# Performance work log

Hardware: AMD Instinct MI355X
Metric: run time of the kernel (lower is better)

## Reference

```python
import jax, jax.numpy as jnp
import numpy as np

B, H, W = 4, 240, 320
J = 2            # BONE_NUM
F = 64           # FEATURE_CHANNELS
R = 32           # voxel RESOLUTION
THRESH = 0.7
BIG = 1e30
# channel layout from init_hp(): nocs | mask | loc | pose | skin | conf | feature
NE = 3
ME = NE + 1
LE = ME + J * 3
PE = LE + J * 3
SE = PE + J + 2
CE = SE + J
FE = CE + F      # = 86 total channels


def _rodrigues(r):
    # axis-angle [..., 3] -> rotation matrix [..., 3, 3]
    ang = jnp.sqrt(jnp.sum(r * r, -1, keepdims=True)) + 1e-8
    ax = r / ang
    x, y, z = ax[..., 0], ax[..., 1], ax[..., 2]
    zz = jnp.zeros_like(x)
    K = jnp.stack([zz, -z, y, z, zz, -x, -y, x, zz], -1).reshape(r.shape[:-1] + (3, 3))
    c = jnp.cos(ang)[..., None]
    s = jnp.sin(ang)[..., None]
    return jnp.eye(3, dtype=r.dtype) + s * K + (1.0 - c) * (K @ K)


def setup_inputs() -> dict:
    key = jax.random.key(0)
    return {"output": jax.random.normal(key, (B, FE, H, W), dtype=jnp.float32)}


def _forward(output):
    mask = jax.nn.sigmoid(output[:, NE])                      # [B,H,W]
    conf = output[:, SE:CE]                                   # [B,J,H,W]
    score = jax.nn.sigmoid(conf) * mask[:, None]
    score = score / (score.reshape(B, J, -1).sum(-1)[:, :, None, None] + 1e-5)

    def vote(jmap):  # weighted joint voting, joint map detached as in torch
        jm = jmap.reshape(B, J, 3, H, W) * mask[:, None, None]
        jm = jax.lax.stop_gradient(jm) * score[:, :, None]
        return jm.reshape(B, J, 3, -1).sum(-1)                # [B,J,3]

    loc = vote(output[:, ME:LE])
    rot = vote(output[:, LE:PE])
    # pad root joint (identity transform) at index 0 -> J+1 joints
    locp = jnp.concatenate([jnp.zeros((B, 1, 3), output.dtype), loc], 1)
    rotp = jnp.concatenate([jnp.zeros((B, 1, 3), output.dtype), rot], 1)
    Rm = _rodrigues(-rotp)                                    # [B,J+1,3,3]
    t = locp[..., None]
    trans = t - Rm @ t                                        # Trans(loc)@Rot@Trans(-loc)
    bottom = jnp.broadcast_to(jnp.array([0, 0, 0, 1], output.dtype), (B, J + 1, 1, 4))
    M = jnp.concatenate([jnp.concatenate([Rm, trans], -1), bottom], -2)  # [B,J+1,4,4]

    # per-pixel hard segmentation one-hot over flags 1..J+1 (flag 0 -> zero transform)
    seg = output[:, PE:SE]                                    # [B,J+2,H,W]
    amax = jnp.argmax(seg, axis=1)                            # [B,H,W]
    oh = (amax[:, None] == jnp.arange(1, J + 2)[None, :, None, None]).astype(output.dtype)
    T = jnp.einsum('bjhw,bjpq->bhwpq', oh, M)                 # [B,H,W,4,4]

    nocs = jnp.moveaxis(output[:, :NE], 1, -1)                # [B,H,W,3]
    homog = jnp.concatenate([nocs, jnp.ones_like(nocs[..., :1])], -1)
    pn = jnp.einsum('bhwpq,bhwq->bhwp', T[..., :3, :], homog) # reposed points [B,H,W,3]

    masked = mask > THRESH
    m4 = masked[..., None]
    low = jnp.where(m4, pn, BIG).min(axis=(1, 2))             # [B,3]
    up = jnp.where(m4, pn, -BIG).max(axis=(1, 2))
    scale = (up - low).max(-1)                                # [B]
    safe = jnp.where(scale == 0, 1.0, scale)[:, None, None, None]
    pn_n = jnp.where((scale != 0)[:, None, None, None], (pn - low[:, None, None]) / safe, pn)
    pn_map = jnp.where(m4, pn_n, 0.0)                         # [B,H,W,3]

    out_cat = jnp.concatenate([output, jnp.moveaxis(pn_map, -1, 1)], axis=1)

    # lift + discretize: scatter per-pixel features of valid points into R^3 grid
    feat = jnp.moveaxis(output[:, CE:FE], 1, -1)              # [B,H,W,F]
    vx = jnp.clip(jnp.floor(pn_map * R).astype(jnp.int32), 0, R - 1)
    flat = vx[..., 0] * R * R + vx[..., 1] * R + vx[..., 2]
    flat = jnp.where(masked, flat, R ** 3)                    # invalid -> dump bin

    def scat(fl, ft):
        g = jnp.zeros((R ** 3 + 1, F), ft.dtype).at[fl.reshape(-1)].add(ft.reshape(-1, F))
        return jnp.moveaxis(g[:R ** 3].reshape(R, R, R, F), -1, 0)

    occ = jax.vmap(scat)(flat, feat)                          # [B,F,R,R,R]
    return out_cat, occ


def reference(output):
    return _forward(output)
```

## Files before the change

kernel.cpp:

```cpp
#include <hip/hip_runtime.h>
#include <math.h>

#define HW     76800
#define HW4    19200
#define NCH    86
#define OCH    89
#define NB     4
#define VOX    32768
#define NBLKV  75
#define THRESHF 0.7f
#define BIGF   1e30f

typedef float f4 __attribute__((ext_vector_type(4)));


__device__ __forceinline__ float sigmoidf_(float x) {
    if (x >= 0.f) { return 1.f / (1.f + expf(-x)); }
    float e = expf(x); return e / (1.f + e);
}
__device__ __forceinline__ unsigned fkey(float f) {
    unsigned u = __float_as_uint(f);
    return (u & 0x80000000u) ? ~u : (u | 0x80000000u);
}
__device__ __forceinline__ float funkey(unsigned k) {
    unsigned u = (k & 0x80000000u) ? (k ^ 0x80000000u) : ~k;
    return __uint_as_float(u);
}
__device__ __forceinline__ int vox1(float q) {
    int v = (int)floorf(q * 32.f);
    return v < 0 ? 0 : (v > 31 ? 31 : v);
}

__global__ __launch_bounds__(256) void k_votes_zero(const f4* __restrict__ in4,
                                                    float* __restrict__ ws,
                                                    f4* __restrict__ zp, unsigned n4) {
    const int b = blockIdx.y, bx = blockIdx.x;
    const int tid = threadIdx.x;

    if (bx >= NBLKV) {
        const int zb = b * NBLKV + (bx - NBLKV);
        unsigned gid = (unsigned)zb * 256u + tid;
        f4 z = {0.f, 0.f, 0.f, 0.f};
        for (unsigned i = gid; i < n4; i += NB * NBLKV * 256u)
            __builtin_nontemporal_store(z, &zp[i]);
        if (gid < NB * 1024) ((unsigned*)(ws + 8192))[gid] = 0u;
        if (zb == 0 && tid < 24) {
            unsigned* keys = (unsigned*)(ws + 256);
            keys[tid] = ((tid % 6) < 3) ? fkey(BIGF) : fkey(-BIGF);
        }
        return;
    }

    const size_t ib = (size_t)b * NCH * HW4 + bx * 256 + tid;
    f4 mv = in4[ib + (size_t)3 * HW4];
    f4 c0 = in4[ib + (size_t)20 * HW4];
    f4 c1 = in4[ib + (size_t)21 * HW4];
    f4 L[12];
#pragma unroll
    for (int i = 0; i < 12; i++) L[i] = in4[ib + (size_t)(4 + i) * HW4];
    float acc[14];
#pragma unroll
    for (int i = 0; i < 14; i++) acc[i] = 0.f;
#pragma unroll
    for (int k = 0; k < 4; k++) {
        float m  = sigmoidf_(mv[k]);
        float s0 = sigmoidf_(c0[k]) * m;
        float s1 = sigmoidf_(c1[k]) * m;
        float w0 = m * s0, w1 = m * s1;
        acc[0] += s0; acc[7] += s1;
#pragma unroll
        for (int c = 0; c < 3; c++) {
            acc[1 + c]  += L[c][k]     * w0;
            acc[8 + c]  += L[3 + c][k] * w1;
            acc[4 + c]  += L[6 + c][k] * w0;
            acc[11 + c] += L[9 + c][k] * w1;
        }
    }
    __shared__ float red[4][14];
    int lane = tid & 63, wid = tid >> 6;
#pragma unroll
    for (int i = 0; i < 14; i++) {
        float v = acc[i];
        for (int off = 32; off > 0; off >>= 1) v += __shfl_down(v, off, 64);
        if (lane == 0) red[wid][i] = v;
    }
    __syncthreads();
    if (tid < 14)
        ws[512 + (b * NBLKV + bx) * 16 + tid] =
            red[0][tid] + red[1][tid] + red[2][tid] + red[3][tid];
}

__global__ __launch_bounds__(256) void k_minmax(const f4* __restrict__ in4,
                                                float* __restrict__ ws) {
    __shared__ float vsh[14];
    __shared__ float Msh[36];
    const int b = blockIdx.y, bx = blockIdx.x, tid = threadIdx.x;
    if (tid < 14) {
        const float* part = ws + 512 + (size_t)b * NBLKV * 16 + tid;
        float s = 0.f;
#pragma unroll 5
        for (int blk = 0; blk < NBLKV; blk++) s += part[blk * 16];
        vsh[tid] = s;
    }
    __syncthreads();
    if (tid < 3) {
        int k = tid;
        float lp0 = 0, lp1 = 0, lp2 = 0, rp0 = 0, rp1 = 0, rp2 = 0;
        if (k > 0) {
            const float* v = vsh + (k - 1) * 7;
            float d = v[0] + 1e-5f;
            lp0 = v[1] / d; lp1 = v[2] / d; lp2 = v[3] / d;
            rp0 = v[4] / d; rp1 = v[5] / d; rp2 = v[6] / d;
        }
        float rx = -rp0, ry = -rp1, rz = -rp2;
        float ang = sqrtf(rx * rx + ry * ry + rz * rz) + 1e-8f;
        float ax = rx / ang, ay = ry / ang, az = rz / ang;
        float K[3][3] = {{0.f, -az, ay}, {az, 0.f, -ax}, {-ay, ax, 0.f}};
        float c = cosf(ang), s = sinf(ang);
        float K2[3][3], Rm[3][3];
#pragma unroll
        for (int i = 0; i < 3; i++)
#pragma unroll
            for (int j = 0; j < 3; j++)
                K2[i][j] = K[i][0] * K[0][j] + K[i][1] * K[1][j] + K[i][2] * K[2][j];
#pragma unroll
        for (int i = 0; i < 3; i++)
#pragma unroll
            for (int j = 0; j < 3; j++)
                Rm[i][j] = (i == j ? 1.f : 0.f) + s * K[i][j] + (1.f - c) * K2[i][j];
#pragma unroll
        for (int i = 0; i < 3; i++) {
            float tt = (i == 0 ? lp0 : (i == 1 ? lp1 : lp2));
            float tr = tt - (Rm[i][0] * lp0 + Rm[i][1] * lp1 + Rm[i][2] * lp2);
            Msh[k * 12 + i * 4 + 0] = Rm[i][0];
            Msh[k * 12 + i * 4 + 1] = Rm[i][1];
            Msh[k * 12 + i * 4 + 2] = Rm[i][2];
            Msh[k * 12 + i * 4 + 3] = tr;
            if (bx == 0) {
                float* M = ws + 64 + (b * 3 + k) * 12;
                M[i * 4 + 0] = Rm[i][0]; M[i * 4 + 1] = Rm[i][1];
                M[i * 4 + 2] = Rm[i][2]; M[i * 4 + 3] = tr;
            }
        }
    }
    __syncthreads();

    const size_t ib = (size_t)b * NCH * HW4 + bx * 256 + tid;
    f4 n0 = in4[ib], n1 = in4[ib + HW4], n2 = in4[ib + 2 * HW4];
    f4 mv = in4[ib + 3 * HW4];
    f4 g0 = in4[ib + 16 * HW4], g1 = in4[ib + 17 * HW4];
    f4 g2 = in4[ib + 18 * HW4], g3 = in4[ib + 19 * HW4];
    float mn[3] = {BIGF, BIGF, BIGF}, mx[3] = {-BIGF, -BIGF, -BIGF};
#pragma unroll
    for (int k = 0; k < 4; k++) {
        float m = sigmoidf_(mv[k]);
        if (!(m > THRESHF)) continue;
        int am = 0; float bb = g0[k];
        if (g1[k] > bb) { bb = g1[k]; am = 1; }
        if (g2[k] > bb) { bb = g2[k]; am = 2; }
        if (g3[k] > bb) { bb = g3[k]; am = 3; }
        float px = 0.f, py = 0.f, pz = 0.f;
        if (am > 0) {
            const float* Mk = Msh + (am - 1) * 12;
            float a = n0[k], bq = n1[k], cq = n2[k];
            px = Mk[0] * a + Mk[1] * bq + Mk[2]  * cq + Mk[3];
            py = Mk[4] * a + Mk[5] * bq + Mk[6]  * cq + Mk[7];
            pz = Mk[8] * a + Mk[9] * bq + Mk[10] * cq + Mk[11];
        }
        mn[0] = fminf(mn[0], px); mn[1] = fminf(mn[1], py); mn[2] = fminf(mn[2], pz);
        mx[0] = fmaxf(mx[0], px); mx[1] = fmaxf(mx[1], py); mx[2] = fmaxf(mx[2], pz);
    }
    __shared__ float rmn[4][3], rmx[4][3];
    int lane = tid & 63, wid = tid >> 6;
#pragma unroll
    for (int i = 0; i < 3; i++) {
        float v = mn[i];
        for (int off = 32; off > 0; off >>= 1) v = fminf(v, __shfl_down(v, off, 64));
        if (lane == 0) rmn[wid][i] = v;
        float u = mx[i];
        for (int off = 32; off > 0; off >>= 1) u = fmaxf(u, __shfl_down(u, off, 64));
        if (lane == 0) rmx[wid][i] = u;
    }
    __syncthreads();
    unsigned* keys = (unsigned*)(ws + 256);
    if (tid < 3) {
        float v = fminf(fminf(rmn[0][tid], rmn[1][tid]), fminf(rmn[2][tid], rmn[3][tid]));
        atomicMin(&keys[b * 6 + tid], fkey(v));
    } else if (tid < 6) {
        int i = tid - 3;
        float v = fmaxf(fmaxf(rmx[0][i], rmx[1][i]), fmaxf(rmx[2][i], rmx[3][i]));
        atomicMax(&keys[b * 6 + 3 + i], fkey(v));
    }
}

template<bool VOXMAJOR>
__global__ __launch_bounds__(256) void k_scatter(const f4* __restrict__ in4,
                                                 f4* __restrict__ out4,
                                                 float* __restrict__ dst,
                                                 float* __restrict__ ws) {
    __shared__ float tile[64][257];
    __shared__ float accz[4][64];
    const int b = blockIdx.y, blk = blockIdx.x;
    const int tid = threadIdx.x, lane = tid & 63, w = tid >> 6;
    const size_t ib4 = (size_t)b * NCH * HW4 + (size_t)blk * 64;
    const size_t ob4 = (size_t)b * OCH * HW4 + (size_t)blk * 64;
    unsigned* bm = (unsigned*)(ws + 8192) + b * 1024;

    const unsigned* keys = (const unsigned*)(ws + 256);
    float l0 = funkey(keys[b * 6 + 0]), l1 = funkey(keys[b * 6 + 1]), l2 = funkey(keys[b * 6 + 2]);
    float u0 = funkey(keys[b * 6 + 3]), u1 = funkey(keys[b * 6 + 4]), u2 = funkey(keys[b * 6 + 5]);
    float scale = fmaxf(u0 - l0, fmaxf(u1 - l1, u2 - l2));
    float safe = (scale == 0.f) ? 1.f : scale;
    bool flag = scale != 0.f;
    float z0 = flag ? (0.f - l0) / safe : 0.f;
    float z1 = flag ? (0.f - l1) / safe : 0.f;
    float z2 = flag ? (0.f - l2) / safe : 0.f;
    const int fl0 = vox1(z0) * 1024 + vox1(z1) * 32 + vox1(z2);

    const float* ibs = (const float*)in4 + (size_t)b * NCH * HW + blk * 256 + tid;
    float* obs = (float*)out4 + (size_t)b * OCH * HW + blk * 256 + tid;
    float n0 = ibs[0], n1 = ibs[(size_t)HW], n2 = ibs[(size_t)2 * HW];
    float mvv = ibs[(size_t)3 * HW];
    float g0 = ibs[(size_t)16 * HW], g1 = ibs[(size_t)17 * HW];
    float g2 = ibs[(size_t)18 * HW], g3 = ibs[(size_t)19 * HW];
    float m = sigmoidf_(mvv);
    bool masked = m > THRESHF;
    int am = 0;
    { float bb = g0;
      if (g1 > bb) { bb = g1; am = 1; }
      if (g2 > bb) { bb = g2; am = 2; }
      if (g3 > bb) { bb = g3; am = 3; } }
    bool glb  = masked && (am != 0);
    bool spec = masked && (am == 0);
    float px = 0.f, py = 0.f, pz = 0.f;
    if (am > 0) {
        const float* Mk = ws + 64 + b * 36 + (am - 1) * 12;
        px = Mk[0] * n0 + Mk[1] * n1 + Mk[2]  * n2 + Mk[3];
        py = Mk[4] * n0 + Mk[5] * n1 + Mk[6]  * n2 + Mk[7];
        pz = Mk[8] * n0 + Mk[9] * n1 + Mk[10] * n2 + Mk[11];
    }
    float qx, qy, qz;
    if (flag) { qx = (px - l0) / safe; qy = (py - l1) / safe; qz = (pz - l2) / safe; }
    else      { qx = px; qy = py; qz = pz; }
    float ox = masked ? qx : 0.f, oy = masked ? qy : 0.f, oz = masked ? qz : 0.f;
    obs[(size_t)86 * HW] = ox;
    obs[(size_t)87 * HW] = oy;
    obs[(size_t)88 * HW] = oz;
    int flat = glb ? (vox1(ox) * 1024 + vox1(oy) * 32 + vox1(oz)) : fl0;
    unsigned long long gm = __ballot(glb);
    unsigned long long sm = __ballot(spec);

#pragma unroll
    for (int i = 0; i < 6; i++) {
        int c = w + 4 * i;
        if (c < 22) {
            f4 v = in4[ib4 + (size_t)c * HW4 + lane];
            out4[ob4 + (size_t)c * HW4 + lane] = v;
        }
    }
#pragma unroll
    for (int i = 0; i < 16; i++) {
        int c = w * 16 + i;
        f4 v = in4[ib4 + (size_t)(22 + c) * HW4 + lane];
        out4[ob4 + (size_t)(22 + c) * HW4 + lane] = v;
        tile[c][4 * lane + 0] = v[0]; tile[c][4 * lane + 1] = v[1];
        tile[c][4 * lane + 2] = v[2]; tile[c][4 * lane + 3] = v[3];
    }
    if (VOXMAJOR && tid == 0 && sm)
        atomicOr(&bm[fl0 >> 5], 1u << (fl0 & 31));
    __syncthreads();

    while (gm) {
        int i0 = __ffsll(gm) - 1;
        int fl = __shfl(flat, i0, 64);
        unsigned long long match = __ballot(flat == fl) & gm;
        gm &= ~match;
        float s = 0.f;
        unsigned long long mm = match;
        while (mm) {
            int j = __ffsll(mm) - 1; mm &= mm - 1;
            s += tile[lane][w * 64 + j];
        }
        if (VOXMAJOR) {
            if (lane == 0) atomicOr(&bm[fl >> 5], 1u << (fl & 31));
            atomicAdd(&dst[(((size_t)b * VOX + fl) << 6) + lane], s);
        } else {
            atomicAdd(&dst[(((size_t)(b * 64 + lane)) << 15) + fl], s);
        }
    }
    float sacc = 0.f;
    while (sm) {
        int j = __ffsll(sm) - 1; sm &= sm - 1;
        sacc += tile[lane][w * 64 + j];
    }
    accz[w][lane] = sacc;
    __syncthreads();
    if (tid < 64) {
        float s = accz[0][tid] + accz[1][tid] + accz[2][tid] + accz[3][tid];
        if (s != 0.f) {
            if (VOXMAJOR)
                atomicAdd(&dst[(((size_t)b * VOX + fl0) << 6) + tid], s);
            else
                atomicAdd(&dst[(((size_t)(b * 64 + tid)) << 15) + fl0], s);
        }
    }
}

__global__ __launch_bounds__(256) void k_transpose(const float* __restrict__ tmp,
                                                   float* __restrict__ occ,
                                                   const float* __restrict__ ws) {
    __shared__ float ld[64][65];
    const int b = blockIdx.y;
    const int vox0 = blockIdx.x * 64;
    const int t = threadIdx.x;
    const unsigned* bm = (const unsigned*)(ws + 8192) + b * 1024;
    const unsigned dirty = bm[vox0 >> 5] | bm[(vox0 >> 5) + 1];
    const int f = t >> 2, sub = t & 3;
    float* dstp = occ + (((size_t)(b * 64 + f)) << 15) + vox0;

    if (dirty == 0u) {
        f4 z = {0.f, 0.f, 0.f, 0.f};
#pragma unroll
        for (int i = 0; i < 4; i++)
            *(f4*)(dstp + 4 * (sub * 4 + i)) = z;
        return;
    }
    const int v = t & 63, g = t >> 6;
    const float* src = tmp + (((size_t)b * VOX + vox0 + v) << 6) + g * 16;
#pragma unroll
    for (int i = 0; i < 4; i++) {
        f4 x = *(const f4*)(src + 4 * i);
        ld[g * 16 + 4 * i + 0][v] = x[0];
        ld[g * 16 + 4 * i + 1][v] = x[1];
        ld[g * 16 + 4 * i + 2][v] = x[2];
        ld[g * 16 + 4 * i + 3][v] = x[3];
    }
    __syncthreads();
#pragma unroll
    for (int i = 0; i < 4; i++) {
        int mq = sub * 4 + i;
        f4 x;
        x[0] = ld[f][4 * mq + 0]; x[1] = ld[f][4 * mq + 1];
        x[2] = ld[f][4 * mq + 2]; x[3] = ld[f][4 * mq + 3];
        *(f4*)(dstp + 4 * mq) = x;
    }
}

extern "C" void kernel_launch(void* const* d_in, const int* in_sizes, int n_in,
                              void* d_out, int out_size, void* d_ws, size_t ws_size,
                              hipStream_t stream) {
    const f4* in4 = (const f4*)d_in[0];
    float* out = (float*)d_out;
    float* ws = (float*)d_ws;
    float* occ = out + (size_t)NB * OCH * HW;
    float* tmp = ws + 32768;
    const size_t tmp_bytes = (size_t)NB * VOX * 64 * sizeof(float);
    const bool voxmajor = ws_size >= 32768 * sizeof(float) + tmp_bytes;
    const unsigned n4 = (unsigned)(tmp_bytes / 16);

    dim3 gv(NBLKV * 2, NB);
    if (voxmajor) k_votes_zero<<<gv, 256, 0, stream>>>(in4, ws, (f4*)tmp, n4);
    else          k_votes_zero<<<gv, 256, 0, stream>>>(in4, ws, (f4*)occ, n4);
    dim3 g75(NBLKV, NB);
    k_minmax<<<g75, 256, 0, stream>>>(in4, ws);
    dim3 gs(300, NB);
    if (voxmajor) {
        k_scatter<true><<<gs, 256, 0, stream>>>(in4, (f4*)out, tmp, ws);
        dim3 gt(VOX / 64, NB);
        k_transpose<<<gt, 256, 0, stream>>>(tmp, occ, ws);
    } else {
        k_scatter<false><<<gs, 256, 0, stream>>>(in4, (f4*)out, occ, ws);
    }
}
```

Baseline: 101.1 us.

## Drop LDS feature tile in scatter; gather features directly from global memory

Removes the 64x257 shared-memory tile and the block-wide barriers from the scatter kernel. Feature sums are now read straight from global memory, where the lines were just loaded and are likely cached. Special-flag pixels now go through the same ballot/match loop as other masked pixels instead of a separate block reduction. This frees LDS, which should raise occupancy and remove the syncs. The cost is scattered strided global loads per match and possibly more atomics on the fl0 bin.

After: 139.6 us. +38.1%, slower.

```diff
diff --git a/kernel.cpp b/kernel.cpp
--- a/kernel.cpp
+++ b/kernel.cpp
@@ -198,8 +198,6 @@
                                                  f4* __restrict__ out4,
                                                  float* __restrict__ dst,
                                                  float* __restrict__ ws) {
-    __shared__ float tile[64][257];
-    __shared__ float accz[4][64];
     const int b = blockIdx.y, blk = blockIdx.x;
     const int tid = threadIdx.x, lane = tid & 63, w = tid >> 6;
     const size_t ib4 = (size_t)b * NCH * HW4 + (size_t)blk * 64;
@@ -230,8 +228,6 @@
       if (g1 > bb) { bb = g1; am = 1; }
       if (g2 > bb) { bb = g2; am = 2; }
       if (g3 > bb) { bb = g3; am = 3; } }
-    bool glb  = masked && (am != 0);
-    bool spec = masked && (am == 0);
     float px = 0.f, py = 0.f, pz = 0.f;
     if (am > 0) {
         const float* Mk = ws + 64 + b * 36 + (am - 1) * 12;
@@ -246,30 +242,23 @@
     obs[(size_t)86 * HW] = ox;
     obs[(size_t)87 * HW] = oy;
     obs[(size_t)88 * HW] = oz;
-    int flat = glb ? (vox1(ox) * 1024 + vox1(oy) * 32 + vox1(oz)) : fl0;
-    unsigned long long gm = __ballot(glb);
-    unsigned long long sm = __ballot(spec);
-
-#pragma unroll
-    for (int i = 0; i < 6; i++) {
-        int c = w + 4 * i;
-        if (c < 22) {
-            f4 v = in4[ib4 + (size_t)c * HW4 + lane];
-            out4[ob4 + (size_t)c * HW4 + lane] = v;
-        }
-    }
-#pragma unroll
+    int flat = masked ? ((am != 0) ? (vox1(ox) * 1024 + vox1(oy) * 32 + vox1(oz)) : fl0)
+                      : -1;
+    unsigned long long gm = __ballot(masked);
+
+    for (int c = w; c < 22; c += 4) {
+        f4 v = in4[ib4 + (size_t)c * HW4 + lane];
+        out4[ob4 + (size_t)c * HW4 + lane] = v;
+    }
+#pragma unroll 4
     for (int i = 0; i < 16; i++) {
-        int c = w * 16 + i;
-        f4 v = in4[ib4 + (size_t)(22 + c) * HW4 + lane];
-        out4[ob4 + (size_t)(22 + c) * HW4 + lane] = v;
-        tile[c][4 * lane + 0] = v[0]; tile[c][4 * lane + 1] = v[1];
-        tile[c][4 * lane + 2] = v[2]; tile[c][4 * lane + 3] = v[3];
-    }
-    if (VOXMAJOR && tid == 0 && sm)
-        atomicOr(&bm[fl0 >> 5], 1u << (fl0 & 31));
-    __syncthreads();
-
+        int c = 22 + w * 16 + i;
+        f4 v = in4[ib4 + (size_t)c * HW4 + lane];
+        out4[ob4 + (size_t)c * HW4 + lane] = v;
+    }
+
+    const float* gsrc = (const float*)in4 + (size_t)b * NCH * HW
+                      + (size_t)(22 + lane) * HW + blk * 256 + w * 64;
     while (gm) {
         int i0 = __ffsll(gm) - 1;
         int fl = __shfl(flat, i0, 64);
@@ -279,29 +268,13 @@
         unsigned long long mm = match;
         while (mm) {
             int j = __ffsll(mm) - 1; mm &= mm - 1;
-            s += tile[lane][w * 64 + j];
+            s += gsrc[j];
         }
         if (VOXMAJOR) {
             if (lane == 0) atomicOr(&bm[fl >> 5], 1u << (fl & 31));
             atomicAdd(&dst[(((size_t)b * VOX + fl) << 6) + lane], s);
         } else {
             atomicAdd(&dst[(((size_t)(b * 64 + lane)) << 15) + fl], s);
-        }
-    }
-    float sacc = 0.f;
-    while (sm) {
-        int j = __ffsll(sm) - 1; sm &= sm - 1;
-        sacc += tile[lane][w * 64 + j];
-    }
-    accz[w][lane] = sacc;
-    __syncthreads();
-    if (tid < 64) {
-        float s = accz[0][tid] + accz[1][tid] + accz[2][tid] + accz[3][tid];
-        if (s != 0.f) {
-            if (VOXMAJOR)
-                atomicAdd(&dst[(((size_t)b * VOX + fl0) << 6) + tid], s);
-            else
-                atomicAdd(&dst[(((size_t)(b * 64 + tid)) << 15) + fl0], s);
         }
     }
 }
```
